# Performance work log

Hardware: AMD Instinct MI355X
Metric: run time of the kernel (lower is better)

The kernel has to match this reference:

```python
import jax, jax.numpy as jnp
import numpy as np

BS, D_IN, D_H, D_Z = 4096, 784, 400, 20


def setup_inputs() -> dict:
    key = jax.random.key(0)
    ks = jax.random.split(key, 13)
    s = 0.05
    return {
        "x": jax.random.normal(ks[0], (BS, D_IN), dtype=jnp.float32),
        "W1": jax.random.normal(ks[1], (D_H, D_IN), dtype=jnp.float32) * s,
        "b1": jax.random.normal(ks[2], (D_H,), dtype=jnp.float32) * s,
        "W21": jax.random.normal(ks[3], (D_Z, D_H), dtype=jnp.float32) * s,
        "b21": jax.random.normal(ks[4], (D_Z,), dtype=jnp.float32) * s,
        "W22": jax.random.normal(ks[5], (D_Z, D_H), dtype=jnp.float32) * s,
        "b22": jax.random.normal(ks[6], (D_Z,), dtype=jnp.float32) * s,
        "W3": jax.random.normal(ks[7], (D_H, D_Z), dtype=jnp.float32) * s,
        "b3": jax.random.normal(ks[8], (D_H,), dtype=jnp.float32) * s,
        "W41": jax.random.normal(ks[9], (D_IN, D_H), dtype=jnp.float32) * s,
        "b41": jax.random.normal(ks[10], (D_IN,), dtype=jnp.float32) * s,
        "W42": jax.random.normal(ks[11], (D_IN, D_H), dtype=jnp.float32) * s,
        "b42": jax.random.normal(ks[12], (D_IN,), dtype=jnp.float32) * s,
    }


def reference(x, W1, b1, W21, b21, W22, b22, W3, b3, W41, b41, W42, b42):
    xr = x.reshape(-1, D_IN)                              # [bs, 784]
    # encode
    h1 = jax.nn.relu(xr @ W1.T + b1)                      # [bs, 400]
    mu = h1 @ W21.T + b21                                 # [bs, 20]
    logvar = h1 @ W22.T + b22                             # [bs, 20]
    # unscented sigma points: varsqrt[:, i] = sqrt(N)*logvar[:, i]*e_i
    N = D_Z
    sqrtN = jnp.asarray(np.sqrt(N), dtype=x.dtype)
    # delta[i, b, j] = sqrt(N) * logvar[b, i] * (i == j)   -> [N, bs, N]
    delta = sqrtN * logvar.T[:, :, None] * jnp.eye(N, dtype=x.dtype)[:, None, :]
    z = jnp.concatenate([mu[None] + delta, mu[None] - delta], axis=0)  # [2N, bs, N]

    def decode(zs):
        h3 = jax.nn.relu(zs @ W3.T + b3)                  # [bs, 400]
        return zs @ W41.T * 0 + (h3 @ W41.T + b41), h3 @ W42.T + b42

    def decode_clean(zs):
        h3 = jax.nn.relu(zs @ W3.T + b3)
        return h3 @ W41.T + b41, h3 @ W42.T + b42

    # original loop decodes every sigma point; recon_x keeps the last one
    mu_x, var_x = jax.vmap(decode_clean)(z)               # each [2N, bs, 784]
    recon_mu = mu_x[-1]
    recon_var = var_x[-1]
    return recon_mu, recon_var, mu, logvar, z
```

## Files before the change

### kernel.cpp

```cpp
#include <hip/hip_runtime.h>
#include <hip/hip_bf16.h>

#define BS   4096
#define DIN  784
#define DH   400
#define DZ   20

#define KPH  416
#define KPD  448

#define OFF_RMU  0
#define OFF_RVAR 3211264
#define OFF_MU   6422528
#define OFF_LV   6504448
#define OFF_Z    6586368

#define WS_WCAT  0
#define WS_W2C   1404928
#define WS_H1B   1444864
#define WS_H3B   4852736

#define SQRT20F 4.47213595499958f

using short8 = __attribute__((ext_vector_type(8))) short;
using f4     = __attribute__((ext_vector_type(4))) float;

__device__ __forceinline__ short bf16r(float f) {
    union { float f; unsigned u; } v; v.f = f;
    unsigned r = (v.u + 0x7fffu + ((v.u >> 16) & 1u)) >> 16;
    return (short)r;
}

__device__ __forceinline__ void glds16(const void* g, void* l) {
    __builtin_amdgcn_global_load_lds(
        (const __attribute__((address_space(1))) unsigned int*)g,
        (__attribute__((address_space(3))) unsigned int*)l,
        16, 0, 0);
}

__global__ __launch_bounds__(256)
void k1(const float* __restrict__ x, const float* __restrict__ W1,
        const float* __restrict__ b1,
        const float* __restrict__ W41, const float* __restrict__ W42,
        const float* __restrict__ W21, const float* __restrict__ W22,
        short* __restrict__ h1b, char* __restrict__ ws) {
    __shared__ short sA[2][64 * 64];
    __shared__ short sB[2][80 * 64];

    const int tid = threadIdx.x;
    const int bid = blockIdx.x;

    if (bid >= 320) {
        short* wcat = (short*)(ws + WS_WCAT);
        short* w2c  = (short*)(ws + WS_W2C);
        const int NC = 1568 * 56 + 48 * 52;
        for (int p = (bid - 320) * 256 + tid; p < NC; p += 64 * 256) {
            const float* sr = nullptr;
            short* dst;
            int c;
            if (p < 1568 * 56) {
                int row = p / 56; c = p - row * 56;
                sr = (row < 784) ? (W41 + (size_t)row * DH)
                                 : (W42 + (size_t)(row - 784) * DH);
                dst = wcat + (size_t)row * KPD + c * 8;
            } else {
                int q = p - 1568 * 56;
                int row = q / 52; c = q - row * 52;
                if (row < 20)      sr = W21 + (size_t)row * DH;
                else if (row < 40) sr = W22 + (size_t)(row - 20) * DH;
                dst = w2c + (size_t)row * KPH + c * 8;
            }
            short8 v;
            if (c < 50 && sr) {
                f4 a = *(const f4*)(sr + c * 8);
                f4 b = *(const f4*)(sr + c * 8 + 4);
#pragma unroll
                for (int e = 0; e < 4; ++e) { v[e] = bf16r(a[e]); v[4 + e] = bf16r(b[e]); }
            } else {
#pragma unroll
                for (int e = 0; e < 8; ++e) v[e] = 0;
            }
            *(short8*)dst = v;
        }
        return;
    }

    const int swz = (bid & 7) * 40 + (bid >> 3);
    const int bm = swz / 5, bn = swz - bm * 5;
    const int w = tid >> 6, l = tid & 63, lg = l >> 4, lr = l & 15;

    f4 acc[5] = {};
    f4 ar[4];
    f4 br[6];

    auto a_load = [&](int kt) {
#pragma unroll
        for (int i = 0; i < 2; ++i) {
            int c = tid + i * 256;
            int row = c >> 3, kc = c & 7;
            int gk = kt * 64 + kc * 8;
            if (gk < DIN) {
                const float* src = x + (size_t)(bm * 64 + row) * DIN + gk;
                ar[2 * i] = *(const f4*)src;
                ar[2 * i + 1] = *(const f4*)(src + 4);
            } else {
                ar[2 * i] = (f4){0.f, 0.f, 0.f, 0.f};
                ar[2 * i + 1] = (f4){0.f, 0.f, 0.f, 0.f};
            }
        }
    };
    auto b_load = [&](int kt) {
#pragma unroll
        for (int i = 0; i < 3; ++i) {
            int c = tid + i * 256;
            if (c < 640) {
                int row = c >> 3, kc = c & 7;
                int gk = kt * 64 + kc * 8;
                if (gk < DIN) {
                    const float* src = W1 + (size_t)(bn * 80 + row) * DIN + gk;
                    br[2 * i] = *(const f4*)src;
                    br[2 * i + 1] = *(const f4*)(src + 4);
                } else {
                    br[2 * i] = (f4){0.f, 0.f, 0.f, 0.f};
                    br[2 * i + 1] = (f4){0.f, 0.f, 0.f, 0.f};
                }
            }
        }
    };
    auto ab_write = [&](int buf) {
#pragma unroll
        for (int i = 0; i < 2; ++i) {
            int c = tid + i * 256;
            int row = c >> 3, kc = c & 7;
            short8 v;
#pragma unroll
            for (int e = 0; e < 4; ++e) { v[e] = bf16r(ar[2 * i][e]); v[4 + e] = bf16r(ar[2 * i + 1][e]); }
            *(short8*)&sA[buf][(row * 8 + (kc ^ (row & 7))) * 8] = v;
        }
#pragma unroll
        for (int i = 0; i < 3; ++i) {
            int c = tid + i * 256;
            if (c < 640) {
                int row = c >> 3, kc = c & 7;
                short8 v;
#pragma unroll
                for (int e = 0; e < 4; ++e) { v[e] = bf16r(br[2 * i][e]); v[4 + e] = bf16r(br[2 * i + 1][e]); }
                *(short8*)&sB[buf][(row * 8 + (kc ^ (row & 7))) * 8] = v;
            }
        }
    };
    auto compute = [&](int buf) {
        const int row = w * 16 + lr;
#pragma unroll
        for (int kk = 0; kk < 2; ++kk) {
            short8 a = *(const short8*)&sA[buf][(row * 8 + ((kk * 4 + lg) ^ (row & 7))) * 8];
#pragma unroll
            for (int ni = 0; ni < 5; ++ni) {
                int brw = ni * 16 + lr;
                short8 b = *(const short8*)&sB[buf][(brw * 8 + ((kk * 4 + lg) ^ (brw & 7))) * 8];
                acc[ni] = __builtin_amdgcn_mfma_f32_16x16x32_bf16(a, b, acc[ni], 0, 0, 0);
            }
        }
    };

    a_load(0); b_load(0); ab_write(0);
    __syncthreads();
    for (int kt = 0; kt < 13; ++kt) {
        const int cur = kt & 1;
        if (kt < 12) { a_load(kt + 1); b_load(kt + 1); }
        compute(cur);
        if (kt < 12) ab_write(cur ^ 1);
        __syncthreads();
    }

#pragma unroll
    for (int ni = 0; ni < 5; ++ni) {
        int col = bn * 80 + ni * 16 + lr;
        float bias = b1[col];
#pragma unroll
        for (int r = 0; r < 4; ++r) {
            int row = bm * 64 + w * 16 + lg * 4 + r;
            float v = acc[ni][r] + bias;
            h1b[(size_t)row * KPH + col] = bf16r(v > 0.f ? v : 0.f);
        }
    }
    if (bn == 4) {
        for (int p = tid; p < 64 * 16; p += 256) {
            int r = p >> 4, c = 400 + (p & 15);
            h1b[(size_t)(bm * 64 + r) * KPH + c] = 0;
        }
    }
}

__global__ __launch_bounds__(256)
void k_mid(const short* __restrict__ h1b, const short* __restrict__ w2c,
           const float* __restrict__ W3, const float* __restrict__ b3,
           const float* __restrict__ b21, const float* __restrict__ b22,
           float* __restrict__ out, short* __restrict__ h3b) {
    __shared__ short sA[16 * 416];
    __shared__ short sB[48 * 416];
    __shared__ short sW[400 * 40];
    __shared__ float muv[2][16][20];
    __shared__ short zl[16 * 40];
    __shared__ short h3s[16 * 448];

    const int tid = threadIdx.x;
    const int blk = blockIdx.x;
    const int w = tid >> 6, l = tid & 63, lg = l >> 4, lr = l & 15;
    const int r0 = blk * 16;

#pragma unroll
    for (int it = 0; it < 4; ++it) {
        int p = it * 256 + tid;
        if (p < 832) {
            int r = p / 52, cp = p - r * 52, c = cp ^ (r & 3);
            glds16(h1b + (size_t)(r0 + r) * KPH + c * 8, &sA[p * 8]);
        }
    }
#pragma unroll
    for (int it = 0; it < 10; ++it) {
        int p = it * 256 + tid;
        if (p < 2496) {
            int r = p / 52, cp = p - r * 52, c = cp ^ (r & 3);
            glds16(w2c + (size_t)r * KPH + c * 8, &sB[p * 8]);
        }
    }
    if (tid < 200) {
#pragma unroll
        for (int i = 0; i < 2; ++i) {
            int r = tid + i * 200;
            const float* src = W3 + (size_t)r * DZ;
            f4 f0 = *(const f4*)src;
            f4 f1 = *(const f4*)(src + 4);
            f4 f2 = *(const f4*)(src + 8);
            f4 f3 = *(const f4*)(src + 12);
            f4 f5 = *(const f4*)(src + 16);
            short8 c0, c1, c2, c3;
#pragma unroll
            for (int e = 0; e < 4; ++e) {
                c0[e] = bf16r(f0[e]); c0[4 + e] = bf16r(f1[e]);
                c1[e] = bf16r(f2[e]); c1[4 + e] = bf16r(f3[e]);
                c2[e] = bf16r(f5[e]); c2[4 + e] = 0;
                c3[e] = 0; c3[4 + e] = 0;
            }
            *(short8*)&sW[r * 40 + 0]  = c0;
            *(short8*)&sW[r * 40 + 8]  = c1;
            *(short8*)&sW[r * 40 + 16] = c2;
            *(short8*)&sW[r * 40 + 24] = c3;
        }
    }
    __syncthreads();

    if (w == 0) {
        f4 a3[3] = {};
#pragma unroll
        for (int kk = 0; kk < 13; ++kk) {
            short8 a = *(const short8*)&sA[(lr * 52 + ((kk * 4 + lg) ^ (lr & 3))) * 8];
#pragma unroll
            for (int ni = 0; ni < 3; ++ni) {
                int br = ni * 16 + lr;
                short8 b = *(const short8*)&sB[(br * 52 + ((kk * 4 + lg) ^ (br & 3))) * 8];
                a3[ni] = __builtin_amdgcn_mfma_f32_16x16x32_bf16(a, b, a3[ni], 0, 0, 0);
            }
        }
#pragma unroll
        for (int ni = 0; ni < 3; ++ni) {
            int n = ni * 16 + lr;
            if (n < 40) {
                float bias = (n < 20) ? b21[n] : b22[n - 20];
#pragma unroll
                for (int r = 0; r < 4; ++r) {
                    int row = lg * 4 + r;
                    float v = a3[ni][r] + bias;
                    if (n < 20) {
                        muv[0][row][n] = v;
                        out[OFF_MU + (size_t)(r0 + row) * 20 + n] = v;
                    } else {
                        muv[1][row][n - 20] = v;
                        out[OFF_LV + (size_t)(r0 + row) * 20 + (n - 20)] = v;
                    }
                }
            }
        }
    }
    __syncthreads();

    if (tid < 80) {
        int row = tid / 5, c = tid - (tid / 5) * 5;
        short8 v;
#pragma unroll
        for (int e = 0; e < 8; ++e) {
            int j = c * 8 + e;
            float val = 0.f;
            if (j < 20) {
                val = muv[0][row][j];
                if (j == 19) val -= SQRT20F * muv[1][row][19];
            }
            v[e] = bf16r(val);
        }
        *(short8*)&zl[row * 40 + c * 8] = v;
    } else if (tid < 176) {
        int t = tid - 80;
        int row = t / 6, c = t - (t / 6) * 6;
        short8 zz;
#pragma unroll
        for (int e = 0; e < 8; ++e) zz[e] = 0;
        *(short8*)&h3s[row * 448 + 400 + c * 8] = zz;
    }
#pragma unroll
    for (int it = 0; it < 13; ++it) {
        int p = it * 256 + tid;
        if (p < 3200) {
            int s = p / 80, q = p - s * 80;
            int row = q / 5, j4 = q - (q / 5) * 5;
            f4 v = *(const f4*)&muv[0][row][j4 * 4];
            int sp = (s < 20) ? s : s - 20;
            if ((sp >> 2) == j4) {
                float add = ((s < 20) ? SQRT20F : -SQRT20F) * muv[1][row][sp];
                int e = sp & 3;
#pragma unroll
                for (int k = 0; k < 4; ++k) v[k] += (e == k) ? add : 0.f;
            }
            *(f4*)(out + OFF_Z + ((size_t)s * BS + r0 + row) * 20 + j4 * 4) = v;
        }
    }
    __syncthreads();

    for (int f = w; f < 25; f += 4) {
        int n0 = f * 16;
        short8 a = *(const short8*)&zl[lr * 40 + lg * 8];
        short8 b = *(const short8*)&sW[(n0 + lr) * 40 + lg * 8];
        f4 z4 = {};
        f4 accv = __builtin_amdgcn_mfma_f32_16x16x32_bf16(a, b, z4, 0, 0, 0);
        int n = n0 + lr;
        float bias = b3[n];
#pragma unroll
        for (int r = 0; r < 4; ++r) {
            int row = lg * 4 + r;
            float v = accv[r] + bias;
            h3s[row * 448 + n] = bf16r(v > 0.f ? v : 0.f);
        }
    }
    __syncthreads();

#pragma unroll
    for (int it = 0; it < 4; ++it) {
        int p = it * 256 + tid;
        if (p < 896) {
            int row = p / 56, c = p - (p / 56) * 56;
            *(short8*)(h3b + (size_t)(r0 + row) * KPD + c * 8) =
                *(const short8*)&h3s[row * 448 + c * 8];
        }
    }
}

__global__ __launch_bounds__(256)
void k_gemm4(const short* __restrict__ h3b, const short* __restrict__ wcat,
             const float* __restrict__ b41, const float* __restrict__ b42,
             float* __restrict__ out) {
    __shared__ short sA[2][64 * 64];
    __shared__ short sB[2][112 * 64];

    const int tid = threadIdx.x;
    const int bid = blockIdx.x;
    const int swz = (bid & 7) * 112 + (bid >> 3);
    const int bm = swz / 14, bn = swz - bm * 14;
    const int w = tid >> 6, l = tid & 63, lg = l >> 4, lr = l & 15;

    f4 acc[7] = {};

    auto stage = [&](int buf, int kt) {
#pragma unroll
        for (int i = 0; i < 2; ++i) {
            int c = tid + i * 256;
            int r = c >> 3, kc = (c & 7) ^ (r & 7);
            glds16(h3b + (size_t)(bm * 64 + r) * KPD + kt * 64 + kc * 8, &sA[buf][c * 8]);
        }
#pragma unroll
        for (int i = 0; i < 4; ++i) {
            int c = tid + i * 256;
            if (c < 896) {
                int r = c >> 3, kc = (c & 7) ^ (r & 7);
                glds16(wcat + (size_t)(bn * 112 + r) * KPD + kt * 64 + kc * 8, &sB[buf][c * 8]);
            }
        }
    };

    stage(0, 0);
    __syncthreads();
    for (int kt = 0; kt < 7; ++kt) {
        const int cur = kt & 1;
        if (kt < 6) stage(cur ^ 1, kt + 1);
        const int arow = w * 16 + lr;
#pragma unroll
        for (int kk = 0; kk < 2; ++kk) {
            short8 a = *(const short8*)&sA[cur][(arow * 8 + ((kk * 4 + lg) ^ (arow & 7))) * 8];
#pragma unroll
            for (int ni = 0; ni < 7; ++ni) {
                int br = ni * 16 + lr;
                short8 b = *(const short8*)&sB[cur][(br * 8 + ((kk * 4 + lg) ^ (br & 7))) * 8];
                acc[ni] = __builtin_amdgcn_mfma_f32_16x16x32_bf16(a, b, acc[ni], 0, 0, 0);
            }
        }
        __syncthreads();
    }

    const bool first = (bn < 7);
#pragma unroll
    for (int ni = 0; ni < 7; ++ni) {
        int colt = bn * 112 + ni * 16 + lr;
        int cc = first ? colt : colt - 784;
        float bias = first ? b41[cc] : b42[cc];
        size_t base = first ? (size_t)OFF_RMU : (size_t)OFF_RVAR;
#pragma unroll
        for (int r = 0; r < 4; ++r) {
            size_t row = (size_t)(bm * 64 + w * 16 + lg * 4 + r);
            out[base + row * DIN + cc] = acc[ni][r] + bias;
        }
    }
}

extern "C" void kernel_launch(void* const* d_in, const int* in_sizes, int n_in,
                              void* d_out, int out_size, void* d_ws, size_t ws_size,
                              hipStream_t stream) {
    const float* x   = (const float*)d_in[0];
    const float* W1  = (const float*)d_in[1];
    const float* b1  = (const float*)d_in[2];
    const float* W21 = (const float*)d_in[3];
    const float* b21 = (const float*)d_in[4];
    const float* W22 = (const float*)d_in[5];
    const float* b22 = (const float*)d_in[6];
    const float* W3  = (const float*)d_in[7];
    const float* b3  = (const float*)d_in[8];
    const float* W41 = (const float*)d_in[9];
    const float* b41 = (const float*)d_in[10];
    const float* W42 = (const float*)d_in[11];
    const float* b42 = (const float*)d_in[12];

    float* out = (float*)d_out;
    char*  ws  = (char*)d_ws;
    const short* wcat = (const short*)(ws + WS_WCAT);
    const short* w2c  = (const short*)(ws + WS_W2C);
    short* h1b = (short*)(ws + WS_H1B);
    short* h3b = (short*)(ws + WS_H3B);

    k1<<<384, 256, 0, stream>>>(x, W1, b1, W41, W42, W21, W22, h1b, ws);
    k_mid<<<256, 256, 0, stream>>>(h1b, w2c, W3, b3, b21, b22, out, h3b);
    k_gemm4<<<896, 256, 0, stream>>>(h3b, wcat, b41, b42, out);
}
```

Measured before the change: 49.11 us.

## Pre-convert W1 to bf16, truncate x conversion, and double M-tile in final GEMM

Adds a separate prep kernel that converts W1 (alongside the decoder and mu/logvar weights) to padded bf16, so k1 can stage W1 tiles straight into LDS with global_load_lds instead of loading fp32 and converting each tile. The x tile is now converted to bf16 by taking the high 16 bits (truncation) instead of round-to-nearest, which makes the conversion cheaper but slightly less accurate. The final decoder GEMM uses 128-row tiles with two MFMA row groups per wave, halving the grid and reusing each B tile twice. The cost is an extra kernel launch plus a serial dependency between the prep kernel and k1.

```diff
diff --git a/kernel.cpp b/kernel.cpp
--- a/kernel.cpp
+++ b/kernel.cpp
@@ -6,6 +6,7 @@
 #define DH   400
 #define DZ   20
 
+#define KP1  832
 #define KPH  416
 #define KPD  448
 
@@ -17,13 +18,15 @@
 
 #define WS_WCAT  0
 #define WS_W2C   1404928
-#define WS_H1B   1444864
-#define WS_H3B   4852736
+#define WS_W1B   1444864
+#define WS_H1B   2110464
+#define WS_H3B   5518336
 
 #define SQRT20F 4.47213595499958f
 
 using short8 = __attribute__((ext_vector_type(8))) short;
 using f4     = __attribute__((ext_vector_type(4))) float;
+using i4     = __attribute__((ext_vector_type(4))) int;
 
 __device__ __forceinline__ short bf16r(float f) {
     union { float f; unsigned u; } v; v.f = f;
@@ -38,60 +41,62 @@
         16, 0, 0);
 }
 
+__global__ void k0(const float* __restrict__ W1, const float* __restrict__ W41,
+                   const float* __restrict__ W42, const float* __restrict__ W21,
+                   const float* __restrict__ W22, char* __restrict__ ws) {
+    const int N0 = 400 * 104;
+    const int N1 = N0 + 1568 * 56;
+    const int N2 = N1 + 48 * 52;
+    int gid = blockIdx.x * 256 + threadIdx.x;
+    if (gid >= N2) return;
+
+    const float* sr = nullptr;
+    short* dst;
+    int c, DC;
+    if (gid < N0) {
+        int row = gid / 104; c = gid - row * 104; DC = 98;
+        sr = W1 + (size_t)row * DIN;
+        dst = (short*)(ws + WS_W1B) + (size_t)row * KP1 + c * 8;
+    } else if (gid < N1) {
+        int p = gid - N0;
+        int row = p / 56; c = p - row * 56; DC = 50;
+        sr = (row < 784) ? (W41 + (size_t)row * DH) : (W42 + (size_t)(row - 784) * DH);
+        dst = (short*)(ws + WS_WCAT) + (size_t)row * KPD + c * 8;
+    } else {
+        int p = gid - N1;
+        int row = p / 52; c = p - row * 52; DC = 50;
+        if (row < 20)      sr = W21 + (size_t)row * DH;
+        else if (row < 40) sr = W22 + (size_t)(row - 20) * DH;
+        else               sr = nullptr;
+        dst = (short*)(ws + WS_W2C) + (size_t)row * KPH + c * 8;
+    }
+    short8 v;
+    if (c < DC && sr) {
+        f4 a = *(const f4*)(sr + c * 8);
+        f4 b = *(const f4*)(sr + c * 8 + 4);
+#pragma unroll
+        for (int e = 0; e < 4; ++e) { v[e] = bf16r(a[e]); v[4 + e] = bf16r(b[e]); }
+    } else {
+#pragma unroll
+        for (int e = 0; e < 8; ++e) v[e] = 0;
+    }
+    *(short8*)dst = v;
+}
+
 __global__ __launch_bounds__(256)
-void k1(const float* __restrict__ x, const float* __restrict__ W1,
-        const float* __restrict__ b1,
-        const float* __restrict__ W41, const float* __restrict__ W42,
-        const float* __restrict__ W21, const float* __restrict__ W22,
-        short* __restrict__ h1b, char* __restrict__ ws) {
+void k1(const float* __restrict__ x, const float* __restrict__ b1,
+        const short* __restrict__ W1b, short* __restrict__ h1b) {
     __shared__ short sA[2][64 * 64];
     __shared__ short sB[2][80 * 64];
 
     const int tid = threadIdx.x;
     const int bid = blockIdx.x;
-
-    if (bid >= 320) {
-        short* wcat = (short*)(ws + WS_WCAT);
-        short* w2c  = (short*)(ws + WS_W2C);
-        const int NC = 1568 * 56 + 48 * 52;
-        for (int p = (bid - 320) * 256 + tid; p < NC; p += 64 * 256) {
-            const float* sr = nullptr;
-            short* dst;
-            int c;
-            if (p < 1568 * 56) {
-                int row = p / 56; c = p - row * 56;
-                sr = (row < 784) ? (W41 + (size_t)row * DH)
-                                 : (W42 + (size_t)(row - 784) * DH);
-                dst = wcat + (size_t)row * KPD + c * 8;
-            } else {
-                int q = p - 1568 * 56;
-                int row = q / 52; c = q - row * 52;
-                if (row < 20)      sr = W21 + (size_t)row * DH;
-                else if (row < 40) sr = W22 + (size_t)(row - 20) * DH;
-                dst = w2c + (size_t)row * KPH + c * 8;
-            }
-            short8 v;
-            if (c < 50 && sr) {
-                f4 a = *(const f4*)(sr + c * 8);
-                f4 b = *(const f4*)(sr + c * 8 + 4);
-#pragma unroll
-                for (int e = 0; e < 4; ++e) { v[e] = bf16r(a[e]); v[4 + e] = bf16r(b[e]); }
-            } else {
-#pragma unroll
-                for (int e = 0; e < 8; ++e) v[e] = 0;
-            }
-            *(short8*)dst = v;
-        }
-        return;
-    }
-
     const int swz = (bid & 7) * 40 + (bid >> 3);
     const int bm = swz / 5, bn = swz - bm * 5;
     const int w = tid >> 6, l = tid & 63, lg = l >> 4, lr = l & 15;
 
     f4 acc[5] = {};
-    f4 ar[4];
-    f4 br[6];
+    i4 ar[4];
 
     auto a_load = [&](int kt) {
 #pragma unroll
@@ -100,52 +105,36 @@
             int row = c >> 3, kc = c & 7;
             int gk = kt * 64 + kc * 8;
             if (gk < DIN) {
-                const float* src = x + (size_t)(bm * 64 + row) * DIN + gk;
-                ar[2 * i] = *(const f4*)src;
-                ar[2 * i + 1] = *(const f4*)(src + 4);
+                const int* src = (const int*)(x + (size_t)(bm * 64 + row) * DIN + gk);
+                ar[2 * i] = *(const i4*)src;
+                ar[2 * i + 1] = *(const i4*)(src + 4);
             } else {
-                ar[2 * i] = (f4){0.f, 0.f, 0.f, 0.f};
-                ar[2 * i + 1] = (f4){0.f, 0.f, 0.f, 0.f};
+                ar[2 * i] = (i4){0, 0, 0, 0};
+                ar[2 * i + 1] = (i4){0, 0, 0, 0};
             }
         }
     };
-    auto b_load = [&](int kt) {
-#pragma unroll
-        for (int i = 0; i < 3; ++i) {
-            int c = tid + i * 256;
-            if (c < 640) {
-                int row = c >> 3, kc = c & 7;
-                int gk = kt * 64 + kc * 8;
-                if (gk < DIN) {
-                    const float* src = W1 + (size_t)(bn * 80 + row) * DIN + gk;
-                    br[2 * i] = *(const f4*)src;
-                    br[2 * i + 1] = *(const f4*)(src + 4);
-                } else {
-                    br[2 * i] = (f4){0.f, 0.f, 0.f, 0.f};
-                    br[2 * i + 1] = (f4){0.f, 0.f, 0.f, 0.f};
-                }
-            }
-        }
-    };
-    auto ab_write = [&](int buf) {
+    auto a_write = [&](int buf) {
 #pragma unroll
         for (int i = 0; i < 2; ++i) {
             int c = tid + i * 256;
             int row = c >> 3, kc = c & 7;
             short8 v;
 #pragma unroll
-            for (int e = 0; e < 4; ++e) { v[e] = bf16r(ar[2 * i][e]); v[4 + e] = bf16r(ar[2 * i + 1][e]); }
+            for (int e = 0; e < 4; ++e) {
+                v[e]     = (short)(((unsigned)ar[2 * i][e]) >> 16);
+                v[4 + e] = (short)(((unsigned)ar[2 * i + 1][e]) >> 16);
+            }
             *(short8*)&sA[buf][(row * 8 + (kc ^ (row & 7))) * 8] = v;
         }
-#pragma unroll
-        for (int i = 0; i < 3; ++i) {
-            int c = tid + i * 256;
-            if (c < 640) {
-                int row = c >> 3, kc = c & 7;
-                short8 v;
-#pragma unroll
-                for (int e = 0; e < 4; ++e) { v[e] = bf16r(br[2 * i][e]); v[4 + e] = bf16r(br[2 * i + 1][e]); }
-                *(short8*)&sB[buf][(row * 8 + (kc ^ (row & 7))) * 8] = v;
+    };
+    auto b_stage = [&](int buf, int kt) {
+#pragma unroll
+        for (int it = 0; it < 3; ++it) {
+            int p = it * 256 + tid;
+            if (p < 640) {
+                int r = p >> 3, kc = (p & 7) ^ (r & 7);
+                glds16(W1b + (size_t)(bn * 80 + r) * KP1 + kt * 64 + kc * 8, &sB[buf][p * 8]);
             }
         }
     };
@@ -163,13 +152,13 @@
         }
     };
 
-    a_load(0); b_load(0); ab_write(0);
+    a_load(0); b_stage(0, 0); a_write(0);
     __syncthreads();
     for (int kt = 0; kt < 13; ++kt) {
         const int cur = kt & 1;
-        if (kt < 12) { a_load(kt + 1); b_load(kt + 1); }
+        if (kt < 12) { a_load(kt + 1); b_stage(cur ^ 1, kt + 1); }
         compute(cur);
-        if (kt < 12) ab_write(cur ^ 1);
+        if (kt < 12) a_write(cur ^ 1);
         __syncthreads();
     }
 
@@ -358,23 +347,23 @@
 void k_gemm4(const short* __restrict__ h3b, const short* __restrict__ wcat,
              const float* __restrict__ b41, const float* __restrict__ b42,
              float* __restrict__ out) {
-    __shared__ short sA[2][64 * 64];
+    __shared__ short sA[2][128 * 64];
     __shared__ short sB[2][112 * 64];
 
     const int tid = threadIdx.x;
     const int bid = blockIdx.x;
-    const int swz = (bid & 7) * 112 + (bid >> 3);
+    const int swz = (bid & 7) * 56 + (bid >> 3);
     const int bm = swz / 14, bn = swz - bm * 14;
     const int w = tid >> 6, l = tid & 63, lg = l >> 4, lr = l & 15;
 
-    f4 acc[7] = {};
+    f4 acc[2][7] = {};
 
     auto stage = [&](int buf, int kt) {
 #pragma unroll
-        for (int i = 0; i < 2; ++i) {
+        for (int i = 0; i < 4; ++i) {
             int c = tid + i * 256;
             int r = c >> 3, kc = (c & 7) ^ (r & 7);
-            glds16(h3b + (size_t)(bm * 64 + r) * KPD + kt * 64 + kc * 8, &sA[buf][c * 8]);
+            glds16(h3b + (size_t)(bm * 128 + r) * KPD + kt * 64 + kc * 8, &sA[buf][c * 8]);
         }
 #pragma unroll
         for (int i = 0; i < 4; ++i) {
@@ -391,15 +380,17 @@
     for (int kt = 0; kt < 7; ++kt) {
         const int cur = kt & 1;
         if (kt < 6) stage(cur ^ 1, kt + 1);
-        const int arow = w * 16 + lr;
+        const int row0 = w * 32 + lr, row1 = w * 32 + 16 + lr;
 #pragma unroll
         for (int kk = 0; kk < 2; ++kk) {
-            short8 a = *(const short8*)&sA[cur][(arow * 8 + ((kk * 4 + lg) ^ (arow & 7))) * 8];
+            short8 a0 = *(const short8*)&sA[cur][(row0 * 8 + ((kk * 4 + lg) ^ (row0 & 7))) * 8];
+            short8 a1 = *(const short8*)&sA[cur][(row1 * 8 + ((kk * 4 + lg) ^ (row1 & 7))) * 8];
 #pragma unroll
             for (int ni = 0; ni < 7; ++ni) {
                 int br = ni * 16 + lr;
                 short8 b = *(const short8*)&sB[cur][(br * 8 + ((kk * 4 + lg) ^ (br & 7))) * 8];
-                acc[ni] = __builtin_amdgcn_mfma_f32_16x16x32_bf16(a, b, acc[ni], 0, 0, 0);
+                acc[0][ni] = __builtin_amdgcn_mfma_f32_16x16x32_bf16(a0, b, acc[0][ni], 0, 0, 0);
+                acc[1][ni] = __builtin_amdgcn_mfma_f32_16x16x32_bf16(a1, b, acc[1][ni], 0, 0, 0);
             }
         }
         __syncthreads();
@@ -407,17 +398,19 @@
 
     const bool first = (bn < 7);
 #pragma unroll
-    for (int ni = 0; ni < 7; ++ni) {
-        int colt = bn * 112 + ni * 16 + lr;
-        int cc = first ? colt : colt - 784;
-        float bias = first ? b41[cc] : b42[cc];
-        size_t base = first ? (size_t)OFF_RMU : (size_t)OFF_RVAR;
-#pragma unroll
-        for (int r = 0; r < 4; ++r) {
-            size_t row = (size_t)(bm * 64 + w * 16 + lg * 4 + r);
-            out[base + row * DIN + cc] = acc[ni][r] + bias;
-        }
-    }
+    for (int mi = 0; mi < 2; ++mi)
+#pragma unroll
+        for (int ni = 0; ni < 7; ++ni) {
+            int colt = bn * 112 + ni * 16 + lr;
+            int cc = first ? colt : colt - 784;
+            float bias = first ? b41[cc] : b42[cc];
+            size_t base = first ? (size_t)OFF_RMU : (size_t)OFF_RVAR;
+#pragma unroll
+            for (int r = 0; r < 4; ++r) {
+                size_t row = (size_t)(bm * 128 + w * 32 + mi * 16 + lg * 4 + r);
+                out[base + row * DIN + cc] = acc[mi][ni][r] + bias;
+            }
+        }
 }
 
 extern "C" void kernel_launch(void* const* d_in, const int* in_sizes, int n_in,
@@ -441,10 +434,12 @@
     char*  ws  = (char*)d_ws;
     const short* wcat = (const short*)(ws + WS_WCAT);
     const short* w2c  = (const short*)(ws + WS_W2C);
+    const short* W1b  = (const short*)(ws + WS_W1B);
     short* h1b = (short*)(ws + WS_H1B);
     short* h3b = (short*)(ws + WS_H3B);
 
-    k1<<<384, 256, 0, stream>>>(x, W1, b1, W41, W42, W21, W22, h1b, ws);
+    k0<<<516, 256, 0, stream>>>(W1, W41, W42, W21, W22, ws);
+    k1<<<320, 256, 0, stream>>>(x, b1, W1b, h1b);
     k_mid<<<256, 256, 0, stream>>>(h1b, w2c, W3, b3, b21, b22, out, h3b);
-    k_gemm4<<<896, 256, 0, stream>>>(h3b, wcat, b41, b42, out);
-}
+    k_gemm4<<<448, 256, 0, stream>>>(h3b, wcat, b41, b42, out);
+}
```

After: 44.98 us. 8.4% less time.
